# Kernel optimization log

Hardware: AMD Instinct MI355X
Metric: run time of the kernel (lower is better)

The kernel has to match this reference:

```python
import jax, jax.numpy as jnp
import numpy as np

B, S, D, H = 2, 2048, 1024, 16
HD = D // H  # head_dim = 64

def setup_inputs() -> dict:
    key = jax.random.key(0)
    ks = jax.random.split(key, 11)
    s = 1.0 / np.sqrt(D)
    return {
        "query_input": jax.random.normal(ks[0], (B, S, D), jnp.float32),
        "key_input":   jax.random.normal(ks[1], (B, S, D), jnp.float32),
        "value_input": jax.random.normal(ks[2], (B, S, D), jnp.float32),
        "Wq": jax.random.normal(ks[3], (D, D), jnp.float32) * s,
        "bq": jnp.zeros((D,), jnp.float32),
        "Wk": jax.random.normal(ks[4], (D, D), jnp.float32) * s,
        "bk": jnp.zeros((D,), jnp.float32),
        "Wv": jax.random.normal(ks[5], (D, D), jnp.float32) * s,
        "bv": jnp.zeros((D,), jnp.float32),
        "Wo": jax.random.normal(ks[6], (D, D), jnp.float32) * s,
        "bo": jnp.zeros((D,), jnp.float32),
    }

def _split_heads(x):
    b, s, _ = x.shape
    return x.reshape(b, s, H, HD).transpose(0, 2, 1, 3)  # [B,H,S,HD]

def reference(query_input, key_input, value_input, Wq, bq, Wk, bk, Wv, bv, Wo, bo):
    q = _split_heads(query_input @ Wq + bq)
    k = _split_heads(key_input @ Wk + bk)
    v = _split_heads(value_input @ Wv + bv)
    scores = jnp.einsum('bhqd,bhkd->bhqk', q, k) / jnp.sqrt(jnp.float32(HD))
    attn = jax.nn.softmax(scores, axis=-1)
    out = jnp.einsum('bhqk,bhkd->bhqd', attn, v)
    out = out.transpose(0, 2, 1, 3).reshape(query_input.shape[0], -1, H * HD)
    return out @ Wo + bo
```

## Files before the change

kernel.cpp:

```cpp
#include <hip/hip_runtime.h>
#include <hip/hip_bf16.h>
#include <math.h>

#define B_  2
#define S_  2048
#define D_  1024
#define H_  16
#define HD_ 64

typedef __bf16  bf16x8   __attribute__((ext_vector_type(8)));
typedef float   floatx4  __attribute__((ext_vector_type(4)));
typedef float   floatx16 __attribute__((ext_vector_type(16)));

#define MFMA16(a, b, c) __builtin_amdgcn_mfma_f32_16x16x32_bf16((a), (b), (c), 0, 0, 0)
#define MFMA32(a, b, c) __builtin_amdgcn_mfma_f32_32x32x16_bf16((a), (b), (c), 0, 0, 0)

#define BARRIER_RAW() asm volatile("s_barrier" ::: "memory")
#define WAITVM(N)     asm volatile("s_waitcnt vmcnt(" #N ")" ::: "memory")

__device__ __forceinline__ void load_lds16(const void* g, void* l) {
    __builtin_amdgcn_global_load_lds(
        (const __attribute__((address_space(1))) unsigned int*)g,
        (__attribute__((address_space(3))) unsigned int*)l, 16, 0, 0);
}

__device__ __forceinline__ unsigned pk_bf16(float a, float b) {
    unsigned r;
    asm("v_cvt_pk_bf16_f32 %0, %1, %2" : "=v"(r) : "v"(a), "v"(b));
    return r;
}

__device__ __forceinline__ float exp2_hw(float x) {
    float r;
    asm("v_exp_f32 %0, %1" : "=v"(r) : "v"(x));
    return r;
}

__global__ __launch_bounds__(256) void prep_k(
    const float* __restrict__ x0, const float* __restrict__ x1, const float* __restrict__ x2,
    __hip_bfloat16* __restrict__ o0, __hip_bfloat16* __restrict__ o1, __hip_bfloat16* __restrict__ o2,
    const float* __restrict__ W0, const float* __restrict__ W1,
    const float* __restrict__ W2, const float* __restrict__ W3,
    __hip_bfloat16* __restrict__ T0, __hip_bfloat16* __restrict__ T1,
    __hip_bfloat16* __restrict__ T2, __hip_bfloat16* __restrict__ T3)
{
    const int y = blockIdx.y;
    const int t = threadIdx.x;
    if (y < 3) {
        const float* src = (y == 0) ? x0 : (y == 1) ? x1 : x2;
        __hip_bfloat16* dst = (y == 0) ? o0 : (y == 1) ? o1 : o2;
        const int i = blockIdx.x * 256 + t;
        const float4* s4 = (const float4*)src;
        const float4 a = s4[2 * i + 0];
        const float4 b = s4[2 * i + 1];
        union { __hip_bfloat16 h[8]; uint4 v; } p;
        p.h[0] = __float2bfloat16(a.x); p.h[1] = __float2bfloat16(a.y);
        p.h[2] = __float2bfloat16(a.z); p.h[3] = __float2bfloat16(a.w);
        p.h[4] = __float2bfloat16(b.x); p.h[5] = __float2bfloat16(b.y);
        p.h[6] = __float2bfloat16(b.z); p.h[7] = __float2bfloat16(b.w);
        ((uint4*)dst)[i] = p.v;
        return;
    }
    if (blockIdx.x >= 256) return;
    const int z = y - 3;
    const float* W = (z == 0) ? W0 : (z == 1) ? W1 : (z == 2) ? W2 : W3;
    __hip_bfloat16* Wt = (z == 0) ? T0 : (z == 1) ? T1 : (z == 2) ? T2 : T3;

    __shared__ float T[64][65];
    const int n0 = (blockIdx.x & 15) * 64, k0 = (blockIdx.x >> 4) * 64;
    #pragma unroll
    for (int i = 0; i < 4; ++i) {
        const int u = t + i * 256;
        const int r = u >> 4, c4 = (u & 15) * 4;
        const float4 v = *(const float4*)(W + (size_t)(k0 + r) * D_ + n0 + c4);
        T[r][c4 + 0] = v.x; T[r][c4 + 1] = v.y; T[r][c4 + 2] = v.z; T[r][c4 + 3] = v.w;
    }
    __syncthreads();
    #pragma unroll
    for (int i = 0; i < 4; ++i) {
        const int u = t + i * 256;
        const int n = u >> 4, c4 = (u & 15) * 4;
        union { __hip_bfloat16 h[4]; uint2 v; } p;
        #pragma unroll
        for (int j = 0; j < 4; ++j) p.h[j] = __float2bfloat16(T[c4 + j][n]);
        *(uint2*)(Wt + (size_t)(n0 + n) * D_ + k0 + c4) = p.v;
    }
}

__global__ __launch_bounds__(256) void gemm_qkv_k(
    const __hip_bfloat16* __restrict__ xq, const __hip_bfloat16* __restrict__ xk,
    const __hip_bfloat16* __restrict__ xv,
    const __hip_bfloat16* __restrict__ WqT, const __hip_bfloat16* __restrict__ WkT,
    const __hip_bfloat16* __restrict__ WvT,
    const float* __restrict__ bq, const float* __restrict__ bk, const float* __restrict__ bv,
    __hip_bfloat16* __restrict__ Qh, __hip_bfloat16* __restrict__ Kh,
    __hip_bfloat16* __restrict__ Vt)
{
    constexpr int K = 1024;
    __shared__ __align__(16) short As0[128][32], As1[128][32], As2[128][32], As3[128][32];
    __shared__ __align__(16) short Bs0[128][32], Bs1[128][32], Bs2[128][32], Bs3[128][32];

    const int z = blockIdx.z;
    const __hip_bfloat16* A  = (z == 0) ? xq  : (z == 1) ? xk  : xv;
    const __hip_bfloat16* Bt = (z == 0) ? WqT : (z == 1) ? WkT : WvT;
    const float* bias        = (z == 0) ? bq  : (z == 1) ? bk  : bv;

    const int t    = threadIdx.x;
    const int lane = t & 63, w = t >> 6;
    const int quad = lane >> 4, l16 = lane & 15;
    const int m0   = blockIdx.x * 128, n0 = blockIdx.y * 128;
    const int wm   = (w >> 1) * 64,    wn = (w & 1) * 64;

    floatx4 acc[4][4] = {};

    auto stage = [&](int k0, short (*As)[32], short (*Bs)[32]) {
        #pragma unroll
        for (int i = 0; i < 2; ++i) {
            const int c = t + i * 256;
            const int m = c >> 2, kq = (c ^ (m >> 1)) & 3;
            load_lds16(A + (size_t)(m0 + m) * K + k0 + kq * 8, &As[0][0] + c * 8);
        }
        #pragma unroll
        for (int i = 0; i < 2; ++i) {
            const int c = t + i * 256;
            const int n = c >> 2, kq = (c ^ (n >> 1)) & 3;
            load_lds16(Bt + (size_t)(n0 + n) * K + k0 + kq * 8, &Bs[0][0] + c * 8);
        }
    };

    auto compute = [&](short (*As)[32], short (*Bs)[32]) {
        bf16x8 af[4], bfr[4];
        #pragma unroll
        for (int mt = 0; mt < 4; ++mt) {
            const int r = wm + mt * 16 + l16;
            af[mt]  = *(const bf16x8*)&As[r][((quad ^ (r >> 1)) & 3) * 8];
        }
        #pragma unroll
        for (int nt = 0; nt < 4; ++nt) {
            const int n = wn + nt * 16 + l16;
            bfr[nt] = *(const bf16x8*)&Bs[n][((quad ^ (n >> 1)) & 3) * 8];
        }
        #pragma unroll
        for (int mt = 0; mt < 4; ++mt)
            #pragma unroll
            for (int nt = 0; nt < 4; ++nt)
                acc[mt][nt] = MFMA16(af[mt], bfr[nt], acc[mt][nt]);
    };

    stage(0,  As0, Bs0);
    stage(32, As1, Bs1);
    stage(64, As2, Bs2);
    WAITVM(8);
    BARRIER_RAW();

    short (*Ac)[32] = As0, (*A1)[32] = As1, (*A2)[32] = As2, (*Ap)[32] = As3;
    short (*Bc)[32] = Bs0, (*B1)[32] = Bs1, (*B2)[32] = Bs2, (*Bp)[32] = Bs3;

    for (int tt = 0; tt < 32; ++tt) {
        if (tt + 3 < 32) stage((tt + 3) * 32, Ap, Bp);
        compute(Ac, Bc);
        if (tt < 29) WAITVM(8);
        else if (tt == 29) WAITVM(4);
        else WAITVM(0);
        BARRIER_RAW();
        short (*ta)[32] = Ac; Ac = A1; A1 = A2; A2 = Ap; Ap = ta;
        short (*tb)[32] = Bc; Bc = B1; B1 = B2; B2 = Bp; Bp = tb;
    }

    if (z != 2) {
        const float oscale = (z == 0) ? 0.125f * 1.44269504088896f : 1.0f;
        __hip_bfloat16* outp = (z == 0) ? Qh : Kh;
        #pragma unroll
        for (int mt = 0; mt < 4; ++mt)
            #pragma unroll
            for (int nt = 0; nt < 4; ++nt) {
                const int gn = n0 + wn + nt * 16 + l16;
                const float bi = bias[gn];
                #pragma unroll
                for (int r = 0; r < 4; ++r) {
                    const int gm = m0 + wm + mt * 16 + quad * 4 + r;
                    const float v = (acc[mt][nt][r] + bi) * oscale;
                    outp[(((size_t)(gm >> 11) * H_ + (gn >> 6)) * S_ + (gm & 2047)) * 64 + (gn & 63)] =
                        __float2bfloat16(v);
                }
            }
    } else {
        #pragma unroll
        for (int mt = 0; mt < 4; ++mt)
            #pragma unroll
            for (int nt = 0; nt < 4; ++nt) {
                const int gn = n0 + wn + nt * 16 + l16;
                const float bi = bias[gn];
                const int gm0 = m0 + wm + mt * 16 + quad * 4;
                union { __hip_bfloat16 h[4]; uint2 u; } pk;
                #pragma unroll
                for (int r = 0; r < 4; ++r) pk.h[r] = __float2bfloat16(acc[mt][nt][r] + bi);
                *(uint2*)(Vt + (((size_t)(gm0 >> 11) * H_ + (gn >> 6)) * 64 + (gn & 63)) * S_ +
                          (gm0 & 2047)) = pk.u;
            }
    }
}

__global__ __launch_bounds__(256) void gemm_oproj_k(
    const __hip_bfloat16* __restrict__ A, const __hip_bfloat16* __restrict__ Bt,
    const float* __restrict__ bias, float* __restrict__ out)
{
    constexpr int K = 1024, N = 1024;
    __shared__ __align__(16) short As0[128][32], As1[128][32], As2[128][32], As3[128][32];
    __shared__ __align__(16) short Bs0[64][32],  Bs1[64][32],  Bs2[64][32],  Bs3[64][32];

    const int t    = threadIdx.x;
    const int lane = t & 63, w = t >> 6;
    const int quad = lane >> 4, l16 = lane & 15;
    const int m0   = blockIdx.x * 128, n0 = blockIdx.y * 64;
    const int wm   = (w >> 1) * 64,    wn = (w & 1) * 32;

    floatx4 acc[4][2] = {};

    auto stage = [&](int k0, short (*As)[32], short (*Bs)[32]) {
        #pragma unroll
        for (int i = 0; i < 2; ++i) {
            const int c = t + i * 256;
            const int m = c >> 2, kq = (c ^ (m >> 1)) & 3;
            load_lds16(A + (size_t)(m0 + m) * K + k0 + kq * 8, &As[0][0] + c * 8);
        }
        {
            const int c = t;
            const int n = c >> 2, kq = (c ^ (n >> 1)) & 3;
            load_lds16(Bt + (size_t)(n0 + n) * K + k0 + kq * 8, &Bs[0][0] + c * 8);
        }
    };

    auto compute = [&](short (*As)[32], short (*Bs)[32]) {
        bf16x8 af[4], bfr[2];
        #pragma unroll
        for (int mt = 0; mt < 4; ++mt) {
            const int r = wm + mt * 16 + l16;
            af[mt]  = *(const bf16x8*)&As[r][((quad ^ (r >> 1)) & 3) * 8];
        }
        #pragma unroll
        for (int nt = 0; nt < 2; ++nt) {
            const int n = wn + nt * 16 + l16;
            bfr[nt] = *(const bf16x8*)&Bs[n][((quad ^ (n >> 1)) & 3) * 8];
        }
        #pragma unroll
        for (int mt = 0; mt < 4; ++mt)
            #pragma unroll
            for (int nt = 0; nt < 2; ++nt)
                acc[mt][nt] = MFMA16(af[mt], bfr[nt], acc[mt][nt]);
    };

    stage(0,  As0, Bs0);
    stage(32, As1, Bs1);
    stage(64, As2, Bs2);
    WAITVM(6);
    BARRIER_RAW();

    short (*Ac)[32] = As0, (*A1)[32] = As1, (*A2)[32] = As2, (*Ap)[32] = As3;
    short (*Bc)[32] = Bs0, (*B1)[32] = Bs1, (*B2)[32] = Bs2, (*Bp)[32] = Bs3;

    for (int tt = 0; tt < 32; ++tt) {
        if (tt + 3 < 32) stage((tt + 3) * 32, Ap, Bp);
        compute(Ac, Bc);
        if (tt < 29) WAITVM(6);
        else if (tt == 29) WAITVM(3);
        else WAITVM(0);
        BARRIER_RAW();
        short (*ta)[32] = Ac; Ac = A1; A1 = A2; A2 = Ap; Ap = ta;
        short (*tb)[32] = Bc; Bc = B1; B1 = B2; B2 = Bp; Bp = tb;
    }

    #pragma unroll
    for (int mt = 0; mt < 4; ++mt)
        #pragma unroll
        for (int nt = 0; nt < 2; ++nt) {
            const int gn = n0 + wn + nt * 16 + l16;
            const float bi = bias[gn];
            #pragma unroll
            for (int r = 0; r < 4; ++r) {
                const int gm = m0 + wm + mt * 16 + quad * 4 + r;
                out[(size_t)gm * N + gn] = acc[mt][nt][r] + bi;
            }
        }
}

union AttnSmem {
    struct { short K0[2][64][64], K1[2][64][64], V0[2][64][64], V1[2][64][64]; } s;
    struct { float O[4][64][33]; float L[4][32]; } c;
};

__global__ __launch_bounds__(512) void attn_mfma_k(
    const __hip_bfloat16* __restrict__ Qh, const __hip_bfloat16* __restrict__ Kh,
    const __hip_bfloat16* __restrict__ Vt, __hip_bfloat16* __restrict__ Ctx)
{
    __shared__ __align__(16) AttnSmem sm;

    const int t    = threadIdx.x;
    const int lane = t & 63, w = t >> 6;
    const int l32  = lane & 31, hi = lane >> 5;
    const int wq   = w & 3, half = w >> 2;
    const int ht   = t & 255;
    const int b = blockIdx.z, h = blockIdx.x;
    const size_t bh = (size_t)b * H_ + h;
    const int q0 = blockIdx.y * 128;
    const int kvbase = half * 16;

    bf16x8 qf[4];
    {
        const __hip_bfloat16* qb = Qh + (bh * S_ + q0 + wq * 32 + l32) * 64 + hi * 8;
        #pragma unroll
        for (int ks = 0; ks < 4; ++ks) qf[ks] = *(const bf16x8*)(qb + ks * 16);
    }

    floatx16 oacc[2] = {};
    float ls = 0.f;

    auto stage = [&](int kt, short (*Ks)[64], short (*Vs)[64]) {
        #pragma unroll
        for (int i = 0; i < 2; ++i) {
            const int c = ht + i * 256;
            const int p = c >> 3, kq = (c ^ p) & 7;
            load_lds16(Kh + (bh * S_ + kt * 64 + p) * 64 + kq * 8, &Ks[0][0] + c * 8);
            load_lds16(Vt + (bh * 64 + p) * S_ + kt * 64 + kq * 8, &Vs[0][0] + c * 8);
        }
    };

    auto mkfrags = [&](const float (&e)[16], bf16x8* fr) {
        #pragma unroll
        for (int k2 = 0; k2 < 2; ++k2) {
            unsigned y0 = pk_bf16(e[8 * k2 + 0], e[8 * k2 + 1]);
            unsigned y1 = pk_bf16(e[8 * k2 + 2], e[8 * k2 + 3]);
            unsigned y2 = pk_bf16(e[8 * k2 + 4], e[8 * k2 + 5]);
            unsigned y3 = pk_bf16(e[8 * k2 + 6], e[8 * k2 + 7]);
            asm volatile("v_permlane32_swap_b32 %0, %1" : "+v"(y0), "+v"(y2));
            asm volatile("v_permlane32_swap_b32 %0, %1" : "+v"(y1), "+v"(y3));
            union { unsigned u[4]; bf16x8 v; } pq;
            pq.u[0] = y0; pq.u[1] = y1; pq.u[2] = y2; pq.u[3] = y3;
            fr[k2] = pq.v;
        }
    };

    auto compute = [&](short (*Ks)[64], short (*Vs)[64]) {
        floatx16 sacc[2] = {};
        __builtin_amdgcn_s_setprio(1);
        #pragma unroll
        for (int a = 0; a < 2; ++a) {
            const int row = a * 32 + l32;
            #pragma unroll
            for (int ks = 0; ks < 4; ++ks) {
                const bf16x8 kf =
                    *(const bf16x8*)&Ks[row][(((ks * 2 + hi) ^ row) & 7) * 8];
                sacc[a] = MFMA32(kf, qf[ks], sacc[a]);
            }
        }
        __builtin_amdgcn_s_setprio(0);

        float e0[16], e1[16];
        #pragma unroll
        for (int r = 0; r < 16; ++r) { e0[r] = exp2_hw(sacc[0][r]); ls += e0[r]; }
        #pragma unroll
        for (int r = 0; r < 16; ++r) { e1[r] = exp2_hw(sacc[1][r]); ls += e1[r]; }

        bf16x8 pa[4];
        mkfrags(e0, &pa[0]);
        mkfrags(e1, &pa[2]);

        __builtin_amdgcn_s_setprio(1);
        #pragma unroll
        for (int nt = 0; nt < 2; ++nt) {
            const int row = nt * 32 + l32;
            #pragma unroll
            for (int f = 0; f < 4; ++f) {
                const bf16x8 vf =
                    *(const bf16x8*)&Vs[row][(((f * 2 + hi) ^ row) & 7) * 8];
                oacc[nt] = MFMA32(pa[f], vf, oacc[nt]);
            }
        }
        __builtin_amdgcn_s_setprio(0);
    };

    stage(kvbase, sm.s.K0[half], sm.s.V0[half]);
    for (int kt = 0; kt < 16; kt += 2) {
        __syncthreads();
        stage(kvbase + kt + 1, sm.s.K1[half], sm.s.V1[half]);
        compute(sm.s.K0[half], sm.s.V0[half]);
        __syncthreads();
        if (kt + 2 < 16) stage(kvbase + kt + 2, sm.s.K0[half], sm.s.V0[half]);
        compute(sm.s.K1[half], sm.s.V1[half]);
    }

    ls += __shfl_xor(ls, 32, 64);

    __syncthreads();
    if (half == 1) {
        #pragma unroll
        for (int nt = 0; nt < 2; ++nt)
            #pragma unroll
            for (int r = 0; r < 16; ++r)
                sm.c.O[wq][lane][nt * 16 + r] = oacc[nt][r];
        if (hi == 0) sm.c.L[wq][l32] = ls;
    }
    __syncthreads();
    if (half == 0) {
        ls += sm.c.L[wq][l32];
        const float inv = 1.0f / ls;
        float den[16];
        #pragma unroll
        for (int r = 0; r < 16; ++r)
            den[r] = __shfl(inv, (r & 3) + 8 * (r >> 2) + 4 * hi, 64);

        #pragma unroll
        for (int nt = 0; nt < 2; ++nt)
            #pragma unroll
            for (int r = 0; r < 16; ++r) {
                const int qrow = q0 + wq * 32 + (r & 3) + 8 * (r >> 2) + 4 * hi;
                const int hd   = nt * 32 + l32;
                const float o  = oacc[nt][r] + sm.c.O[wq][lane][nt * 16 + r];
                Ctx[((size_t)b * S_ + qrow) * D_ + h * 64 + hd] =
                    __float2bfloat16(o * den[r]);
            }
    }
}

extern "C" void kernel_launch(void* const* d_in, const int* in_sizes, int n_in,
                              void* d_out, int out_size, void* d_ws, size_t ws_size,
                              hipStream_t stream)
{
    const float* xq = (const float*)d_in[0];
    const float* xk = (const float*)d_in[1];
    const float* xv = (const float*)d_in[2];
    const float* Wq = (const float*)d_in[3];
    const float* bq = (const float*)d_in[4];
    const float* Wk = (const float*)d_in[5];
    const float* bk = (const float*)d_in[6];
    const float* Wv = (const float*)d_in[7];
    const float* bv = (const float*)d_in[8];
    const float* Wo = (const float*)d_in[9];
    const float* bo = (const float*)d_in[10];
    float* out = (float*)d_out;

    const size_t n = (size_t)B_ * S_ * D_;
    char* p = (char*)d_ws;
    __hip_bfloat16* xqb = (__hip_bfloat16*)p;            p += n * 2;
    __hip_bfloat16* xkb = (__hip_bfloat16*)p;            p += n * 2;
    __hip_bfloat16* xvb = (__hip_bfloat16*)p;            p += n * 2;
    __hip_bfloat16* WqT = (__hip_bfloat16*)p;            p += (size_t)D_ * D_ * 2;
    __hip_bfloat16* WkT = (__hip_bfloat16*)p;            p += (size_t)D_ * D_ * 2;
    __hip_bfloat16* WvT = (__hip_bfloat16*)p;            p += (size_t)D_ * D_ * 2;
    __hip_bfloat16* WoT = (__hip_bfloat16*)p;            p += (size_t)D_ * D_ * 2;
    __hip_bfloat16* Qh  = (__hip_bfloat16*)p;            p += n * 2;
    __hip_bfloat16* Kh  = (__hip_bfloat16*)p;            p += n * 2;
    __hip_bfloat16* Vth = (__hip_bfloat16*)p;            p += n * 2;
    __hip_bfloat16* Ctx = (__hip_bfloat16*)p;            p += n * 2;

    prep_k<<<dim3((int)(n / 8 / 256), 7), dim3(256), 0, stream>>>(
        xq, xk, xv, xqb, xkb, xvb, Wq, Wk, Wv, Wo, WqT, WkT, WvT, WoT);

    gemm_qkv_k<<<dim3((B_ * S_) / 128, D_ / 128, 3), dim3(256), 0, stream>>>(
        xqb, xkb, xvb, WqT, WkT, WvT, bq, bk, bv, Qh, Kh, Vth);

    attn_mfma_k<<<dim3(H_, S_ / 128, B_), dim3(512), 0, stream>>>(Qh, Kh, Vth, Ctx);

    gemm_oproj_k<<<dim3((B_ * S_) / 128, D_ / 64), dim3(256), 0, stream>>>(
        Ctx, WoT, bo, out);
}
```

Measured before the change: 225.3 us.

## Fuse fp32-to-bf16 activation cast into QKV GEMM A-tile loads

Removes the separate activation cast pass from the prep kernel. The QKV GEMM now reads fp32 activations straight into registers, converts them to bf16 and writes them to LDS, which avoids writing and re-reading three bf16 copies of the inputs. In exchange the A-operand pipeline drops from 4-stage async global-to-LDS loads to a 2-stage register-staged double buffer with __syncthreads. Each A tile now pulls twice as many bytes, since it is fp32, and may be re-read by up to 8 N-tile blocks, which risks exposing more latency.

After: 236.0 us. 4.8% more time.

```diff
diff --git a/kernel.cpp b/kernel.cpp
--- a/kernel.cpp
+++ b/kernel.cpp
@@ -15,9 +15,6 @@
 #define MFMA16(a, b, c) __builtin_amdgcn_mfma_f32_16x16x32_bf16((a), (b), (c), 0, 0, 0)
 #define MFMA32(a, b, c) __builtin_amdgcn_mfma_f32_32x32x16_bf16((a), (b), (c), 0, 0, 0)
 
-#define BARRIER_RAW() asm volatile("s_barrier" ::: "memory")
-#define WAITVM(N)     asm volatile("s_waitcnt vmcnt(" #N ")" ::: "memory")
-
 __device__ __forceinline__ void load_lds16(const void* g, void* l) {
     __builtin_amdgcn_global_load_lds(
         (const __attribute__((address_space(1))) unsigned int*)g,
@@ -36,38 +33,19 @@
     return r;
 }
 
-__global__ __launch_bounds__(256) void prep_k(
-    const float* __restrict__ x0, const float* __restrict__ x1, const float* __restrict__ x2,
-    __hip_bfloat16* __restrict__ o0, __hip_bfloat16* __restrict__ o1, __hip_bfloat16* __restrict__ o2,
+__global__ __launch_bounds__(256) void transpose4_cast_k(
     const float* __restrict__ W0, const float* __restrict__ W1,
     const float* __restrict__ W2, const float* __restrict__ W3,
     __hip_bfloat16* __restrict__ T0, __hip_bfloat16* __restrict__ T1,
     __hip_bfloat16* __restrict__ T2, __hip_bfloat16* __restrict__ T3)
 {
-    const int y = blockIdx.y;
-    const int t = threadIdx.x;
-    if (y < 3) {
-        const float* src = (y == 0) ? x0 : (y == 1) ? x1 : x2;
-        __hip_bfloat16* dst = (y == 0) ? o0 : (y == 1) ? o1 : o2;
-        const int i = blockIdx.x * 256 + t;
-        const float4* s4 = (const float4*)src;
-        const float4 a = s4[2 * i + 0];
-        const float4 b = s4[2 * i + 1];
-        union { __hip_bfloat16 h[8]; uint4 v; } p;
-        p.h[0] = __float2bfloat16(a.x); p.h[1] = __float2bfloat16(a.y);
-        p.h[2] = __float2bfloat16(a.z); p.h[3] = __float2bfloat16(a.w);
-        p.h[4] = __float2bfloat16(b.x); p.h[5] = __float2bfloat16(b.y);
-        p.h[6] = __float2bfloat16(b.z); p.h[7] = __float2bfloat16(b.w);
-        ((uint4*)dst)[i] = p.v;
-        return;
-    }
-    if (blockIdx.x >= 256) return;
-    const int z = y - 3;
+    const int z = blockIdx.z;
     const float* W = (z == 0) ? W0 : (z == 1) ? W1 : (z == 2) ? W2 : W3;
     __hip_bfloat16* Wt = (z == 0) ? T0 : (z == 1) ? T1 : (z == 2) ? T2 : T3;
 
     __shared__ float T[64][65];
-    const int n0 = (blockIdx.x & 15) * 64, k0 = (blockIdx.x >> 4) * 64;
+    const int t  = threadIdx.x;
+    const int n0 = blockIdx.x * 64, k0 = blockIdx.y * 64;
     #pragma unroll
     for (int i = 0; i < 4; ++i) {
         const int u = t + i * 256;
@@ -88,8 +66,8 @@
 }
 
 __global__ __launch_bounds__(256) void gemm_qkv_k(
-    const __hip_bfloat16* __restrict__ xq, const __hip_bfloat16* __restrict__ xk,
-    const __hip_bfloat16* __restrict__ xv,
+    const float* __restrict__ xq, const float* __restrict__ xk,
+    const float* __restrict__ xv,
     const __hip_bfloat16* __restrict__ WqT, const __hip_bfloat16* __restrict__ WkT,
     const __hip_bfloat16* __restrict__ WvT,
     const float* __restrict__ bq, const float* __restrict__ bk, const float* __restrict__ bv,
@@ -97,11 +75,11 @@
     __hip_bfloat16* __restrict__ Vt)
 {
     constexpr int K = 1024;
-    __shared__ __align__(16) short As0[128][32], As1[128][32], As2[128][32], As3[128][32];
-    __shared__ __align__(16) short Bs0[128][32], Bs1[128][32], Bs2[128][32], Bs3[128][32];
+    __shared__ __align__(16) short As0[128][32], As1[128][32];
+    __shared__ __align__(16) short Bs0[128][32], Bs1[128][32];
 
     const int z = blockIdx.z;
-    const __hip_bfloat16* A  = (z == 0) ? xq  : (z == 1) ? xk  : xv;
+    const float* A           = (z == 0) ? xq  : (z == 1) ? xk  : xv;
     const __hip_bfloat16* Bt = (z == 0) ? WqT : (z == 1) ? WkT : WvT;
     const float* bias        = (z == 0) ? bq  : (z == 1) ? bk  : bv;
 
@@ -113,13 +91,31 @@
 
     floatx4 acc[4][4] = {};
 
-    auto stage = [&](int k0, short (*As)[32], short (*Bs)[32]) {
+    float4 ra[4];
+    auto loadA = [&](int k0) {
         #pragma unroll
         for (int i = 0; i < 2; ++i) {
             const int c = t + i * 256;
             const int m = c >> 2, kq = (c ^ (m >> 1)) & 3;
-            load_lds16(A + (size_t)(m0 + m) * K + k0 + kq * 8, &As[0][0] + c * 8);
-        }
+            const float* src = A + (size_t)(m0 + m) * K + k0 + kq * 8;
+            ra[2 * i + 0] = *(const float4*)(src);
+            ra[2 * i + 1] = *(const float4*)(src + 4);
+        }
+    };
+    auto writeA = [&](short (*As)[32]) {
+        #pragma unroll
+        for (int i = 0; i < 2; ++i) {
+            const int c = t + i * 256;
+            union { __hip_bfloat16 h[8]; uint4 v; } p;
+            const float4 a = ra[2 * i + 0], b = ra[2 * i + 1];
+            p.h[0] = __float2bfloat16(a.x); p.h[1] = __float2bfloat16(a.y);
+            p.h[2] = __float2bfloat16(a.z); p.h[3] = __float2bfloat16(a.w);
+            p.h[4] = __float2bfloat16(b.x); p.h[5] = __float2bfloat16(b.y);
+            p.h[6] = __float2bfloat16(b.z); p.h[7] = __float2bfloat16(b.w);
+            *(uint4*)((char*)&As[0][0] + (size_t)c * 16) = p.v;
+        }
+    };
+    auto stageB = [&](int k0, short (*Bs)[32]) {
         #pragma unroll
         for (int i = 0; i < 2; ++i) {
             const int c = t + i * 256;
@@ -147,24 +143,22 @@
                 acc[mt][nt] = MFMA16(af[mt], bfr[nt], acc[mt][nt]);
     };
 
-    stage(0,  As0, Bs0);
-    stage(32, As1, Bs1);
-    stage(64, As2, Bs2);
-    WAITVM(8);
-    BARRIER_RAW();
-
-    short (*Ac)[32] = As0, (*A1)[32] = As1, (*A2)[32] = As2, (*Ap)[32] = As3;
-    short (*Bc)[32] = Bs0, (*B1)[32] = Bs1, (*B2)[32] = Bs2, (*Bp)[32] = Bs3;
-
-    for (int tt = 0; tt < 32; ++tt) {
-        if (tt + 3 < 32) stage((tt + 3) * 32, Ap, Bp);
+    loadA(0);
+    stageB(0, Bs0);
+    writeA(As0);
+    __syncthreads();
+
+    short (*Ac)[32] = As0, (*Aa)[32] = As1;
+    short (*Bc)[32] = Bs0, (*Ba)[32] = Bs1;
+
+    for (int k0 = 0; k0 < K; k0 += 32) {
+        const bool more = (k0 + 32) < K;
+        if (more) { loadA(k0 + 32); stageB(k0 + 32, Ba); }
         compute(Ac, Bc);
-        if (tt < 29) WAITVM(8);
-        else if (tt == 29) WAITVM(4);
-        else WAITVM(0);
-        BARRIER_RAW();
-        short (*ta)[32] = Ac; Ac = A1; A1 = A2; A2 = Ap; Ap = ta;
-        short (*tb)[32] = Bc; Bc = B1; B1 = B2; B2 = Bp; Bp = tb;
+        if (more) writeA(Aa);
+        __syncthreads();
+        short (*ta)[32] = Ac; Ac = Aa; Aa = ta;
+        short (*tb)[32] = Bc; Bc = Ba; Ba = tb;
     }
 
     if (z != 2) {
@@ -200,6 +194,9 @@
             }
     }
 }
+
+#define BARRIER_RAW() asm volatile("s_barrier" ::: "memory")
+#define WAITVM(N)     asm volatile("s_waitcnt vmcnt(" #N ")" ::: "memory")
 
 __global__ __launch_bounds__(256) void gemm_oproj_k(
     const __hip_bfloat16* __restrict__ A, const __hip_bfloat16* __restrict__ Bt,
@@ -441,9 +438,6 @@
 
     const size_t n = (size_t)B_ * S_ * D_;
     char* p = (char*)d_ws;
-    __hip_bfloat16* xqb = (__hip_bfloat16*)p;            p += n * 2;
-    __hip_bfloat16* xkb = (__hip_bfloat16*)p;            p += n * 2;
-    __hip_bfloat16* xvb = (__hip_bfloat16*)p;            p += n * 2;
     __hip_bfloat16* WqT = (__hip_bfloat16*)p;            p += (size_t)D_ * D_ * 2;
     __hip_bfloat16* WkT = (__hip_bfloat16*)p;            p += (size_t)D_ * D_ * 2;
     __hip_bfloat16* WvT = (__hip_bfloat16*)p;            p += (size_t)D_ * D_ * 2;
@@ -453,11 +447,11 @@
     __hip_bfloat16* Vth = (__hip_bfloat16*)p;            p += n * 2;
     __hip_bfloat16* Ctx = (__hip_bfloat16*)p;            p += n * 2;
 
-    prep_k<<<dim3((int)(n / 8 / 256), 7), dim3(256), 0, stream>>>(
-        xq, xk, xv, xqb, xkb, xvb, Wq, Wk, Wv, Wo, WqT, WkT, WvT, WoT);
+    transpose4_cast_k<<<dim3(16, 16, 4), dim3(256), 0, stream>>>(
+        Wq, Wk, Wv, Wo, WqT, WkT, WvT, WoT);
 
     gemm_qkv_k<<<dim3((B_ * S_) / 128, D_ / 128, 3), dim3(256), 0, stream>>>(
-        xqb, xkb, xvb, WqT, WkT, WvT, bq, bk, bv, Qh, Kh, Vth);
+        xq, xk, xv, WqT, WkT, WvT, bq, bk, bv, Qh, Kh, Vth);
 
     attn_mfma_k<<<dim3(H_, S_ / 128, B_), dim3(512), 0, stream>>>(Qh, Kh, Vth, Ctx);
 
```
